# Kernel tuning notes

Hardware: AMD Instinct MI355X
Metric: run time of the kernel (lower is better)

## Reference

```python
import jax, jax.numpy as jnp
import numpy as np


def setup_inputs() -> dict:
    key = jax.random.key(0)
    k1, k2 = jax.random.split(key)
    b, c, n = 16, 64, 65536
    features = jax.random.normal(k1, (b, c, n), dtype=jnp.float32)
    coords = jax.random.normal(k2, (b, 3, n), dtype=jnp.float32)  # roughly in [-1,1], clamp handles outliers
    return {"features": features, "coords": coords, "resolution": 32}


def reference(features, coords, resolution):
    r = int(resolution)
    r2, r3 = r * r, r * r * r
    b, c, n = features.shape
    # scale_pvcnn path: map coords from [-1,1] to voxel space, clamp, round
    norm_coords = jnp.clip(((coords + 1.0) / 2.0) * r, 0.0, r - 1)
    vox_coords = jnp.round(norm_coords).astype(jnp.int32)
    # linear voxel index per point: [b, n]
    indices = vox_coords[:, 0] * r2 + vox_coords[:, 1] * r + vox_coords[:, 2]
    # append ones channel for counting
    feat1 = jnp.concatenate(
        [features, jnp.ones((b, 1, n), dtype=features.dtype)], axis=1
    )  # [b, c+1, n]

    def scatter_one(f, idx):  # f: [c+1, n], idx: [n]
        return jnp.zeros((c + 1, r3), dtype=f.dtype).at[:, idx].add(f)

    out = jax.vmap(scatter_one)(feat1, indices)  # [b, c+1, r^3]
    cnt = out[:, -1:, :]
    cnt = jnp.where(cnt == 0, jnp.asarray(1e-5, cnt.dtype), cnt)
    vox_feature = (out[:, :-1, :] / cnt).reshape(b, c, r, r, r)
    return vox_feature, norm_coords
```

## Files before the change

kernel.cpp:

```cpp
#include <hip/hip_runtime.h>

constexpr int Rr = 32;
constexpr int R2 = Rr * Rr;
constexpr int R3 = Rr * Rr * Rr;
constexpr int Bb = 16;
constexpr int Cc = 64;
constexpr int Nn = 65536;
constexpr int VOX_ELEMS = Bb * Cc * R3;
constexpr int NCELL = Bb * R3;

__device__ __forceinline__ unsigned pack_bf16(float a, float b)
{
    unsigned ua = __float_as_uint(a);
    unsigned ub = __float_as_uint(b);
    ua += 0x7FFFu + ((ua >> 16) & 1u);
    ub += 0x7FFFu + ((ub >> 16) & 1u);
    return (ua >> 16) | (ub & 0xFFFF0000u);
}

__global__ __launch_bounds__(256) void zero_cnt_kernel(float4* __restrict__ base)
{
    int i = blockIdx.x * 256 + threadIdx.x;
    base[i] = float4{0.0f, 0.0f, 0.0f, 0.0f};
}

__global__ __launch_bounds__(256) void vox_coords_kernel(
    const float* __restrict__ coords,
    float* __restrict__ norm_out,
    int* __restrict__ idx_out,
    int* __restrict__ cnt)
{
    int t = blockIdx.x * 256 + threadIdx.x;
    int b = t >> 16;
    int i = t & (Nn - 1);

    const float* cp = coords + (size_t)b * 3 * Nn + i;
    float x = cp[0];
    float y = cp[Nn];
    float z = cp[2 * Nn];

    float nx = fminf(fmaxf((x + 1.0f) * 16.0f, 0.0f), 31.0f);
    float ny = fminf(fmaxf((y + 1.0f) * 16.0f, 0.0f), 31.0f);
    float nz = fminf(fmaxf((z + 1.0f) * 16.0f, 0.0f), 31.0f);

    float* np_ = norm_out + (size_t)b * 3 * Nn + i;
    np_[0]      = nx;
    np_[Nn]     = ny;
    np_[2 * Nn] = nz;

    int idx = (int)rintf(nx) * R2 + (int)rintf(ny) * Rr + (int)rintf(nz);

    int k = atomicAdd(&cnt[(b << 15) + idx], 1);
    idx_out[t] = (idx << 3) | min(k, 7);
}

__global__ __launch_bounds__(256) void slot3zero_kernel(
    const int* __restrict__ cnt, unsigned short* __restrict__ voxT4)
{
    int g = blockIdx.x * 256 + threadIdx.x;
    int cell = g >> 3;
    int p    = g & 7;
    if (cnt[cell] > 4)
        *(float4*)(voxT4 + ((size_t)cell << 8) + 192 + (p << 3)) =
            float4{0.0f, 0.0f, 0.0f, 0.0f};
}

__global__ __launch_bounds__(256) void tscatter_store_kernel(
    const float* __restrict__ feat,
    const int* __restrict__ idx_ws,
    const int* __restrict__ cnt,
    unsigned short* __restrict__ voxT4)
{
    __shared__ float lds[64 * 65];
    __shared__ int   dest_sm[64];
    __shared__ int   at_sm[64];
    int b    = blockIdx.x >> 10;
    int tile = blockIdx.x & 1023;
    int n0   = tile << 6;
    int t    = threadIdx.x;

    if (t < 64) {
        int e    = idx_ws[(b << 16) + n0 + t];
        int cell = (b << 15) + (e >> 3);
        int k    = e & 7;
        int cn   = cnt[cell];
        dest_sm[t] = (cell << 8) + (min(k, 3) << 6);
        at_sm[t]   = (k >= 3 && cn > 4) ? 1 : 0;
    }

#pragma unroll
    for (int q = 0; q < 4; ++q) {
        int c  = (t >> 4) + (q << 4);
        int n4 = (t & 15) << 2;
        float4 v = *(const float4*)(feat + (((size_t)(b * Cc + c)) << 16) + n0 + n4);
        lds[(n4 + 0) * 65 + c] = v.x;
        lds[(n4 + 1) * 65 + c] = v.y;
        lds[(n4 + 2) * 65 + c] = v.z;
        lds[(n4 + 3) * 65 + c] = v.w;
    }
    __syncthreads();

    int wave = t >> 6, lane = t & 63;
    int hi = lane >> 5;
    int m  = lane & 31;
#pragma unroll
    for (int kk = 0; kk < 8; ++kk) {
        int n = (wave << 4) + (kk << 1) + hi;
        float f0 = lds[n * 65 + (m << 1) + 0];
        float f1 = lds[n * 65 + (m << 1) + 1];
        unsigned pk = pack_bf16(f0, f1);
        unsigned short* addr = voxT4 + (size_t)dest_sm[n] + (m << 1);
        if (at_sm[n]) {
            asm volatile("global_atomic_pk_add_bf16 %0, %1, off"
                         :: "v"(addr), "v"(pk) : "memory");
        } else {
            *(unsigned*)addr = pk;
        }
    }
}

__global__ __launch_bounds__(256) void merge_transpose_kernel(
    const unsigned short* __restrict__ voxT4,
    const int* __restrict__ cnt,
    float* __restrict__ vox)
{
    __shared__ float lds[64 * 65];
    int b    = blockIdx.x >> 9;
    int tile = blockIdx.x & 511;
    int v0   = tile << 6;
    int t    = threadIdx.x;
    int cl   = t >> 2;
    int q    = t & 3;

    int cell = (b << 15) + v0 + cl;
    int cn   = cnt[cell];

    const unsigned short* base = voxT4 + ((size_t)cell << 8) + (q << 4);

    uint4 wa[4], wb[4];
#pragma unroll
    for (int k = 0; k < 4; ++k) {
        if (k < cn) {
            wa[k] = *(const uint4*)(base + (k << 6));
            wb[k] = *(const uint4*)(base + (k << 6) + 8);
        } else {
            wa[k] = uint4{0u, 0u, 0u, 0u};
            wb[k] = uint4{0u, 0u, 0u, 0u};
        }
    }

    float acc[16];
#pragma unroll
    for (int j = 0; j < 16; ++j) acc[j] = 0.0f;

#pragma unroll
    for (int k = 0; k < 4; ++k) {
        const unsigned* w = &wa[k].x;
#pragma unroll
        for (int j = 0; j < 4; ++j) {
            acc[2 * j + 0] += __uint_as_float(w[j] << 16);
            acc[2 * j + 1] += __uint_as_float(w[j] & 0xFFFF0000u);
        }
        const unsigned* w2 = &wb[k].x;
#pragma unroll
        for (int j = 0; j < 4; ++j) {
            acc[8 + 2 * j + 0] += __uint_as_float(w2[j] << 16);
            acc[8 + 2 * j + 1] += __uint_as_float(w2[j] & 0xFFFF0000u);
        }
    }

    float inv = cn ? 1.0f / (float)cn : 0.0f;
#pragma unroll
    for (int j = 0; j < 16; ++j)
        lds[cl * 65 + (q << 4) + j] = acc[j] * inv;
    __syncthreads();

    int wave = t >> 6, lane = t & 63;
#pragma unroll
    for (int k = 0; k < 16; ++k) {
        int c = (wave << 4) + k;
        vox[(((size_t)(b * Cc + c)) << 15) + v0 + lane] = lds[lane * 65 + c];
    }
}

extern "C" void kernel_launch(void* const* d_in, const int* in_sizes, int n_in,
                              void* d_out, int out_size, void* d_ws, size_t ws_size,
                              hipStream_t stream)
{
    const float* features = (const float*)d_in[0];
    const float* coords   = (const float*)d_in[1];

    float* out      = (float*)d_out;
    float* vox      = out;
    float* norm_out = out + VOX_ELEMS;

    char* ws = (char*)d_ws;
    int*            cnt    = (int*)ws;            ws += (size_t)NCELL * 4;
    int*            idx_ws = (int*)ws;            ws += (size_t)Bb * Nn * 4;
    unsigned short* voxT4  = (unsigned short*)ws;

    zero_cnt_kernel<<<NCELL * 4 / 16 / 256, 256, 0, stream>>>((float4*)cnt);
    vox_coords_kernel<<<(Bb * Nn) / 256, 256, 0, stream>>>(coords, norm_out, idx_ws, cnt);
    slot3zero_kernel<<<NCELL * 8 / 256, 256, 0, stream>>>(cnt, voxT4);
    tscatter_store_kernel<<<Bb * 1024, 256, 0, stream>>>(features, idx_ws, cnt, voxT4);
    merge_transpose_kernel<<<Bb * 512, 256, 0, stream>>>(voxT4, cnt, vox);
}
```

Baseline: 225.7 us.

## Replace slotted bf16 atomic scatter with counting-sort binning via prefix scan

Per-cell counts now feed a three-kernel exclusive prefix scan, and a binning pass assigns each point a contiguous slot. Point features are then written as packed bf16 rows into a cell-sorted buffer with plain stores. The merge kernel reduces each cell's contiguous run instead of four fixed slots plus an overflow slot that used bf16 atomics. This removes the packed-bf16 atomics and the slot-zeroing pass, and it makes crowded cells sum exactly. The cost is extra kernel launches, a single-block serial scan, a second atomic pass over the points, and a variable-length serial loop for crowded cells in the merge.

```diff
diff --git a/kernel.cpp b/kernel.cpp
--- a/kernel.cpp
+++ b/kernel.cpp
@@ -7,7 +7,8 @@
 constexpr int Cc = 64;
 constexpr int Nn = 65536;
 constexpr int VOX_ELEMS = Bb * Cc * R3;
-constexpr int NCELL = Bb * R3;
+constexpr int NCELL  = Bb * R3;
+constexpr int NSLOTS = Bb * Nn;
 
 __device__ __forceinline__ unsigned pack_bf16(float a, float b)
 {
@@ -50,43 +51,80 @@
 
     int idx = (int)rintf(nx) * R2 + (int)rintf(ny) * Rr + (int)rintf(nz);
 
-    int k = atomicAdd(&cnt[(b << 15) + idx], 1);
-    idx_out[t] = (idx << 3) | min(k, 7);
-}
-
-__global__ __launch_bounds__(256) void slot3zero_kernel(
-    const int* __restrict__ cnt, unsigned short* __restrict__ voxT4)
-{
-    int g = blockIdx.x * 256 + threadIdx.x;
-    int cell = g >> 3;
-    int p    = g & 7;
-    if (cnt[cell] > 4)
-        *(float4*)(voxT4 + ((size_t)cell << 8) + 192 + (p << 3)) =
-            float4{0.0f, 0.0f, 0.0f, 0.0f};
-}
-
-__global__ __launch_bounds__(256) void tscatter_store_kernel(
+    idx_out[t] = idx;
+    atomicAdd(&cnt[(b << 15) + idx], 1);
+}
+
+__global__ __launch_bounds__(256) void scan1_kernel(
+    const int* __restrict__ cnt, int* __restrict__ cursor, int* __restrict__ bsums)
+{
+    __shared__ int sm[256];
+    int t = blockIdx.x * 256 + threadIdx.x;
+    int v = cnt[t];
+    sm[threadIdx.x] = v;
+    __syncthreads();
+#pragma unroll
+    for (int off = 1; off < 256; off <<= 1) {
+        int x = (threadIdx.x >= off) ? sm[threadIdx.x - off] : 0;
+        __syncthreads();
+        sm[threadIdx.x] += x;
+        __syncthreads();
+    }
+    cursor[t] = sm[threadIdx.x] - v;
+    if (threadIdx.x == 255) bsums[blockIdx.x] = sm[255];
+}
+
+__global__ __launch_bounds__(256) void scan2_kernel(int* __restrict__ bsums)
+{
+    __shared__ int sm[256];
+    int carry = 0;
+    for (int chunk = 0; chunk < 2048; chunk += 256) {
+        int v = bsums[chunk + threadIdx.x];
+        sm[threadIdx.x] = v;
+        __syncthreads();
+#pragma unroll
+        for (int off = 1; off < 256; off <<= 1) {
+            int x = (threadIdx.x >= off) ? sm[threadIdx.x - off] : 0;
+            __syncthreads();
+            sm[threadIdx.x] += x;
+            __syncthreads();
+        }
+        bsums[chunk + threadIdx.x] = carry + sm[threadIdx.x] - v;
+        carry += sm[255];
+        __syncthreads();
+    }
+}
+
+__global__ __launch_bounds__(256) void scan3_kernel(
+    int* __restrict__ cursor, const int* __restrict__ bsums)
+{
+    int t = blockIdx.x * 256 + threadIdx.x;
+    cursor[t] += bsums[blockIdx.x];
+}
+
+__global__ __launch_bounds__(256) void bin_kernel(
+    int* __restrict__ slotbuf, int* __restrict__ cursor)
+{
+    int t = blockIdx.x * 256 + threadIdx.x;
+    int b = t >> 16;
+    int idx = slotbuf[t];
+    int slot = atomicAdd(&cursor[(b << 15) + idx], 1);
+    slotbuf[t] = slot;
+}
+
+__global__ __launch_bounds__(256) void tscatter_kernel(
     const float* __restrict__ feat,
-    const int* __restrict__ idx_ws,
-    const int* __restrict__ cnt,
-    unsigned short* __restrict__ voxT4)
+    const int* __restrict__ slotbuf,
+    unsigned short* __restrict__ featS)
 {
     __shared__ float lds[64 * 65];
-    __shared__ int   dest_sm[64];
-    __shared__ int   at_sm[64];
+    __shared__ int   slot_sm[64];
     int b    = blockIdx.x >> 10;
     int tile = blockIdx.x & 1023;
     int n0   = tile << 6;
     int t    = threadIdx.x;
 
-    if (t < 64) {
-        int e    = idx_ws[(b << 16) + n0 + t];
-        int cell = (b << 15) + (e >> 3);
-        int k    = e & 7;
-        int cn   = cnt[cell];
-        dest_sm[t] = (cell << 8) + (min(k, 3) << 6);
-        at_sm[t]   = (k >= 3 && cn > 4) ? 1 : 0;
-    }
+    if (t < 64) slot_sm[t] = slotbuf[(b << 16) + n0 + t];
 
 #pragma unroll
     for (int q = 0; q < 4; ++q) {
@@ -108,19 +146,13 @@
         int n = (wave << 4) + (kk << 1) + hi;
         float f0 = lds[n * 65 + (m << 1) + 0];
         float f1 = lds[n * 65 + (m << 1) + 1];
-        unsigned pk = pack_bf16(f0, f1);
-        unsigned short* addr = voxT4 + (size_t)dest_sm[n] + (m << 1);
-        if (at_sm[n]) {
-            asm volatile("global_atomic_pk_add_bf16 %0, %1, off"
-                         :: "v"(addr), "v"(pk) : "memory");
-        } else {
-            *(unsigned*)addr = pk;
-        }
+        *(unsigned*)(featS + ((size_t)slot_sm[n] << 6) + (m << 1)) = pack_bf16(f0, f1);
     }
 }
 
 __global__ __launch_bounds__(256) void merge_transpose_kernel(
-    const unsigned short* __restrict__ voxT4,
+    const unsigned short* __restrict__ featS,
+    const int* __restrict__ cursor,
     const int* __restrict__ cnt,
     float* __restrict__ vox)
 {
@@ -132,10 +164,11 @@
     int cl   = t >> 2;
     int q    = t & 3;
 
-    int cell = (b << 15) + v0 + cl;
-    int cn   = cnt[cell];
-
-    const unsigned short* base = voxT4 + ((size_t)cell << 8) + (q << 4);
+    int cell  = (b << 15) + v0 + cl;
+    int cn    = cnt[cell];
+    int start = cursor[cell] - cn;
+
+    const unsigned short* base = featS + ((size_t)start << 6) + (q << 4);
 
     uint4 wa[4], wb[4];
 #pragma unroll
@@ -169,6 +202,23 @@
         }
     }
 
+    for (int k = 4; k < cn; ++k) {
+        uint4 w0 = *(const uint4*)(base + (k << 6));
+        uint4 w1 = *(const uint4*)(base + (k << 6) + 8);
+        const unsigned* w = &w0.x;
+#pragma unroll
+        for (int j = 0; j < 4; ++j) {
+            acc[2 * j + 0] += __uint_as_float(w[j] << 16);
+            acc[2 * j + 1] += __uint_as_float(w[j] & 0xFFFF0000u);
+        }
+        const unsigned* w2 = &w1.x;
+#pragma unroll
+        for (int j = 0; j < 4; ++j) {
+            acc[8 + 2 * j + 0] += __uint_as_float(w2[j] << 16);
+            acc[8 + 2 * j + 1] += __uint_as_float(w2[j] & 0xFFFF0000u);
+        }
+    }
+
     float inv = cn ? 1.0f / (float)cn : 0.0f;
 #pragma unroll
     for (int j = 0; j < 16; ++j)
@@ -195,13 +245,18 @@
     float* norm_out = out + VOX_ELEMS;
 
     char* ws = (char*)d_ws;
-    int*            cnt    = (int*)ws;            ws += (size_t)NCELL * 4;
-    int*            idx_ws = (int*)ws;            ws += (size_t)Bb * Nn * 4;
-    unsigned short* voxT4  = (unsigned short*)ws;
+    int*            cnt     = (int*)ws;            ws += (size_t)NCELL * 4;
+    int*            cursor  = (int*)ws;            ws += (size_t)NCELL * 4;
+    int*            slotbuf = (int*)ws;            ws += (size_t)NSLOTS * 4;
+    int*            bsums   = (int*)ws;            ws += 2048 * 4;
+    unsigned short* featS   = (unsigned short*)ws;
 
     zero_cnt_kernel<<<NCELL * 4 / 16 / 256, 256, 0, stream>>>((float4*)cnt);
-    vox_coords_kernel<<<(Bb * Nn) / 256, 256, 0, stream>>>(coords, norm_out, idx_ws, cnt);
-    slot3zero_kernel<<<NCELL * 8 / 256, 256, 0, stream>>>(cnt, voxT4);
-    tscatter_store_kernel<<<Bb * 1024, 256, 0, stream>>>(features, idx_ws, cnt, voxT4);
-    merge_transpose_kernel<<<Bb * 512, 256, 0, stream>>>(voxT4, cnt, vox);
-}
+    vox_coords_kernel<<<(Bb * Nn) / 256, 256, 0, stream>>>(coords, norm_out, slotbuf, cnt);
+    scan1_kernel<<<NCELL / 256, 256, 0, stream>>>(cnt, cursor, bsums);
+    scan2_kernel<<<1, 256, 0, stream>>>(bsums);
+    scan3_kernel<<<NCELL / 256, 256, 0, stream>>>(cursor, bsums);
+    bin_kernel<<<(Bb * Nn) / 256, 256, 0, stream>>>(slotbuf, cursor);
+    tscatter_kernel<<<Bb * 1024, 256, 0, stream>>>(features, slotbuf, featS);
+    merge_transpose_kernel<<<Bb * 512, 256, 0, stream>>>(featS, cursor, cnt, vox);
+}
```

Result: slower. 546.5 us (+142.1%).
